# Optimization experiments

Measured on AMD Instinct MI355X. Metric: run time of the kernel, lower is better.

Reference implementation:

```python
import jax, jax.numpy as jnp
import numpy as np

HEAD_SIZE = 64


def setup_inputs() -> dict:
    key = jax.random.key(0)
    k1, k2, k3, k4 = jax.random.split(key, 4)
    B, T, C = 4, 4096, 1024
    x = jax.random.normal(k1, (B, T, C), dtype=jnp.float32)
    s = 1.0 / np.sqrt(C)  # ~kaiming-uniform scale for Linear weights
    Wk = jax.random.normal(k2, (C, HEAD_SIZE), dtype=jnp.float32) * s
    Wq = jax.random.normal(k3, (C, HEAD_SIZE), dtype=jnp.float32) * s
    Wv = jax.random.normal(k4, (C, HEAD_SIZE), dtype=jnp.float32) * s
    return {"x": x, "Wk": Wk, "Wq": Wq, "Wv": Wv}


def reference(x, Wk, Wq, Wv):
    # x: [B,T,C]; Wk/Wq/Wv: [C,H]
    B, T, C = x.shape
    H = Wk.shape[1]
    k = jnp.einsum('btc,ch->bth', x, Wk)
    q = jnp.einsum('btc,ch->bth', x, Wq)
    v = jnp.einsum('btc,ch->bth', x, Wv)
    scale = 1.0 / jnp.sqrt(jnp.asarray(H, dtype=x.dtype))
    scores = jnp.einsum('bqh,bkh->bqk', q, k) * scale  # [B,T,T]
    causal = jnp.tril(jnp.ones((T, T), dtype=bool))
    scores = jnp.where(causal, scores, jnp.asarray(-jnp.inf, dtype=scores.dtype))
    attn = jax.nn.softmax(scores, axis=-1)
    out = jnp.einsum('bqk,bkh->bqh', attn, v)  # [B,T,H]
    return out
```

## Files before the change

kernel.cpp:

```cpp
#include <hip/hip_runtime.h>
#include <hip/hip_bf16.h>

#define T_ 4096
#define C_ 1024
#define H_ 64
#define LSTR 72
#define XBS 1032

typedef short bf16x8 __attribute__((ext_vector_type(8)));
typedef float f32x4 __attribute__((ext_vector_type(4)));

__device__ __forceinline__ short f2bf(float f) {
  union { __hip_bfloat16 h; short s; } u;
  u.h = __float2bfloat16(f);
  return u.s;
}
__device__ __forceinline__ unsigned pack2(float a, float b) {
  return ((unsigned)(unsigned short)f2bf(b) << 16) | (unsigned short)f2bf(a);
}

__device__ __forceinline__ void stage16(const __hip_bfloat16* g,
                                        __hip_bfloat16* l) {
  __builtin_amdgcn_global_load_lds(
      (const __attribute__((address_space(1))) unsigned*)g,
      (__attribute__((address_space(3))) unsigned*)l, 16, 0, 0);
}

__global__ void wtrans_kernel(const float* __restrict__ Wk,
                              const float* __restrict__ Wq,
                              const float* __restrict__ Wv,
                              __hip_bfloat16* __restrict__ Wtf) {
  int tid = blockIdx.x * 256 + threadIdx.x;
  const int j = tid & 7;
  const int lane = (tid >> 3) & 63;
  const int m = lane & 15;
  const int quad = lane >> 4;
  const int f = (tid >> 9) & 15;
  const int nt = f & 3;
  const int ks = f >> 2;
  const int c = (tid >> 13) & 7;
  const int which = tid >> 16;
  const float* W = (which == 0) ? Wk : ((which == 1) ? Wq : Wv);
  const int cc = c * 128 + ks * 32 + quad * 8 + j;
  const int h = nt * 16 + m;
  Wtf[tid] = __float2bfloat16(W[cc * 64 + h]);
}

__global__ __launch_bounds__(256) void proj_kernel(
    const float* __restrict__ x, const __hip_bfloat16* __restrict__ Wtf,
    __hip_bfloat16* __restrict__ qb, __hip_bfloat16* __restrict__ Kf,
    __hip_bfloat16* __restrict__ Vf) {
  __shared__ __hip_bfloat16 Xb[16 * XBS];
  const int tid = threadIdx.x;
  const int lane = tid & 63;
  const int wave = tid >> 6;
  const int m = lane & 15;
  const int quad = lane >> 4;
  const int t0 = blockIdx.x * 16;

  const float4* xtile = (const float4*)(x + (size_t)t0 * C_);
  float4 xv[16];
#pragma unroll
  for (int k = 0; k < 16; ++k) xv[k] = xtile[tid + k * 256];
#pragma unroll
  for (int k = 0; k < 16; ++k) {
    const int idx = tid + k * 256;
    const int row = idx >> 8;
    const int c4 = idx & 255;
    uint2 u = {pack2(xv[k].x, xv[k].y), pack2(xv[k].z, xv[k].w)};
    *(uint2*)(&Xb[row * XBS + c4 * 4]) = u;
  }
  __syncthreads();

  int whichs[3], ntls[3];
  const __hip_bfloat16* wb[3];
#pragma unroll
  for (int i = 0; i < 3; ++i) {
    const int g = wave * 3 + i;
    whichs[i] = g >> 2;
    ntls[i] = g & 3;
    wb[i] = Wtf + (size_t)whichs[i] * 65536 + ntls[i] * 512 + lane * 8;
  }
  f32x4 acc[3];
#pragma unroll
  for (int i = 0; i < 3; ++i) acc[i] = (f32x4){0.f, 0.f, 0.f, 0.f};

#pragma unroll
  for (int c = 0; c < 8; ++c) {
    bf16x8 bq[12];
#pragma unroll
    for (int i = 0; i < 3; ++i)
#pragma unroll
      for (int ks = 0; ks < 4; ++ks)
        bq[i * 4 + ks] = *(const bf16x8*)(wb[i] + (c * 16 + ks * 4) * 512);
#pragma unroll
    for (int ks = 0; ks < 4; ++ks) {
      bf16x8 a = *(const bf16x8*)(&Xb[m * XBS + c * 128 + ks * 32 + quad * 8]);
#pragma unroll
      for (int i = 0; i < 3; ++i)
        acc[i] = __builtin_amdgcn_mfma_f32_16x16x32_bf16(a, bq[i * 4 + ks],
                                                         acc[i], 0, 0, 0);
    }
  }

  const int bb = t0 >> 12;
  const int tloc = t0 & (T_ - 1);
  const int ktile = tloc >> 6;
  const float cscale = 0.18033688011112042f;

#pragma unroll
  for (int i = 0; i < 3; ++i) {
    const int which = whichs[i];
    const int ntl = ntls[i];
    if (which == 1) {
#pragma unroll
      for (int r = 0; r < 4; ++r)
        qb[(size_t)(t0 + quad * 4 + r) * H_ + ntl * 16 + m] =
            __float2bfloat16(acc[i][r] * cscale);
    } else if (which == 0) {
      __hip_bfloat16* dst = Kf + ((size_t)bb * 64 + ktile) * 4096;
      const int ntK = (tloc >> 4) & 3;
      const int wh = ntl >> 1;
      const int quadK = (ntl * 2 + (m >> 3)) & 3;
      const int j = m & 7;
#pragma unroll
      for (int r = 0; r < 4; ++r) {
        const int mK = quad * 4 + r;
        dst[(ntK * 2 + wh) * 512 + (quadK * 16 + mK) * 8 + j] =
            __float2bfloat16(acc[i][r]);
      }
    } else {
      __hip_bfloat16* dst = Vf + ((size_t)bb * 64 + ktile) * 4096;
#pragma unroll
      for (int r = 0; r < 4; ++r) {
        const int kvo = (tloc & 63) + quad * 4 + r;
        const int half = (kvo >> 5) & 1;
        const int quadV = (kvo >> 3) & 3;
        const int j = kvo & 7;
        dst[(ntl * 2 + half) * 512 + (quadV * 16 + m) * 8 + j] =
            __float2bfloat16(acc[i][r]);
      }
    }
  }
}

__global__ __launch_bounds__(256, 4) void fa_pass1(
    const __hip_bfloat16* __restrict__ qg, const __hip_bfloat16* __restrict__ Kf,
    const __hip_bfloat16* __restrict__ Vf, float* __restrict__ Opart,
    float* __restrict__ Ml) {
  __shared__ __align__(16) __hip_bfloat16 KV[8192];
  __shared__ __hip_bfloat16 Pl[4][16 * LSTR];
  const int lane = threadIdx.x & 63;
  const int wave = threadIdx.x >> 6;
  const int m = lane & 15;
  const int quad = lane >> 4;

  const int sid = 1151 - (int)blockIdx.x;
  const int b = sid / 288;
  const int rem = sid - b * 288;
  int g = 7;
  while (4 * g * (g + 1) > rem) --g;
  const int t = rem - 4 * g * (g + 1);
  const int qq = t / (g + 1);
  const int c = t - qq * (g + 1);
  const int Q = 8 * g + qq;
  const int qt = 4 * Q + wave;
  const int q0 = qt * 16;
  const int jid = b * 1152 + 16 * g * (g + 1) + (4 * qq + wave) * (g + 1) + c;
  const int kt0 = 8 * c;
  const int kcR = Q - 8 * c + 1;
  const int kcount = (kcR < 8) ? kcR : 8;

  const __hip_bfloat16* qbase = qg + ((size_t)b * T_ + q0 + m) * H_;
  bf16x8 qf0 = *(const bf16x8*)(qbase + quad * 8);
  bf16x8 qf1 = *(const bf16x8*)(qbase + 32 + quad * 8);

  f32x4 Oacc[4];
#pragma unroll
  for (int i = 0; i < 4; ++i) Oacc[i] = (f32x4){0.f, 0.f, 0.f, 0.f};
  float psum = 0.f;

  const __hip_bfloat16* Kb = Kf + (size_t)b * 262144;
  const __hip_bfloat16* Vb = Vf + (size_t)b * 262144;
  __hip_bfloat16* Plw = &Pl[wave][0];

  for (int it = 0; it < kcount; ++it) {
    const int ktile = kt0 + it;
    const int k0 = ktile * 64;
    const __hip_bfloat16* kp = Kb + (size_t)ktile * 4096;
    const __hip_bfloat16* vp = Vb + (size_t)ktile * 4096;

    __syncthreads();
#pragma unroll
    for (int i = 0; i < 4; ++i) {
      const int idx = wave * 4 + i;
      const __hip_bfloat16* src =
          (idx < 8) ? (kp + idx * 512) : (vp + (idx - 8) * 512);
      stage16(src + lane * 8, &KV[idx * 512]);
    }
    __syncthreads();

    f32x4 s[4];
#pragma unroll
    for (int nt = 0; nt < 4; ++nt) {
      bf16x8 kf0 = *(const bf16x8*)(&KV[nt * 1024 + lane * 8]);
      bf16x8 kf1 = *(const bf16x8*)(&KV[nt * 1024 + 512 + lane * 8]);
      f32x4 tt = (f32x4){0.f, 0.f, 0.f, 0.f};
      tt = __builtin_amdgcn_mfma_f32_16x16x32_bf16(kf0, qf0, tt, 0, 0, 0);
      tt = __builtin_amdgcn_mfma_f32_16x16x32_bf16(kf1, qf1, tt, 0, 0, 0);
      s[nt] = tt;
    }
    bf16x8 vf[8];
#pragma unroll
    for (int nt = 0; nt < 4; ++nt) {
      vf[2 * nt] = *(const bf16x8*)(&KV[4096 + nt * 1024 + lane * 8]);
      vf[2 * nt + 1] = *(const bf16x8*)(&KV[4096 + nt * 1024 + 512 + lane * 8]);
    }

    const bool needmask = (k0 + 63 > q0);
#pragma unroll
    for (int nt = 0; nt < 4; ++nt) {
      float p[4];
#pragma unroll
      for (int r = 0; r < 4; ++r) {
        float sv = s[nt][r];
        if (needmask && (k0 + nt * 16 + quad * 4 + r) > (q0 + m))
          sv = -__builtin_inff();
        p[r] = exp2f(sv);
        psum += p[r];
      }
      uint2 u = {pack2(p[0], p[1]), pack2(p[2], p[3])};
      *(uint2*)(&Plw[m * LSTR + nt * 16 + quad * 4]) = u;
    }

    bf16x8 pf0 = *(const bf16x8*)(&Plw[m * LSTR + quad * 8]);
    bf16x8 pf1 = *(const bf16x8*)(&Plw[m * LSTR + 32 + quad * 8]);
#pragma unroll
    for (int nt = 0; nt < 4; ++nt) {
      Oacc[nt] = __builtin_amdgcn_mfma_f32_16x16x32_bf16(pf0, vf[2 * nt], Oacc[nt], 0, 0, 0);
      Oacc[nt] = __builtin_amdgcn_mfma_f32_16x16x32_bf16(pf1, vf[2 * nt + 1], Oacc[nt], 0, 0, 0);
    }
  }

  psum += __shfl_xor(psum, 16);
  psum += __shfl_xor(psum, 32);

  float* Op = Opart + (size_t)jid * 1024;
#pragma unroll
  for (int nt = 0; nt < 4; ++nt)
#pragma unroll
    for (int r = 0; r < 4; ++r)
      Op[(quad * 4 + r) * 64 + nt * 16 + m] = Oacc[nt][r];
  if (lane < 16) Ml[(size_t)jid * 16 + lane] = psum;
}

__global__ __launch_bounds__(256) void fa_combine(
    const float* __restrict__ Opart, const float* __restrict__ Ml,
    float* __restrict__ out) {
  const int bq = blockIdx.x;
  const int b = bq >> 8;
  const int qt = bq & 255;
  const int g = qt >> 5;
  const int nc = g + 1;
  const int jbase = b * 1152 + 16 * g * (g + 1) + (qt & 31) * nc;
  const int r = threadIdx.x >> 4;
  const int h0 = (threadIdx.x & 15) * 4;

  float4 O = {0.f, 0.f, 0.f, 0.f};
  float L = 0.f;
  for (int c = 0; c < nc; ++c) {
    L += Ml[(size_t)(jbase + c) * 16 + r];
    float4 o = *(const float4*)(Opart + (size_t)(jbase + c) * 1024 + r * 64 + h0);
    O.x += o.x; O.y += o.y; O.z += o.z; O.w += o.w;
  }
  float inv = 1.f / L;
  float4 res = {O.x * inv, O.y * inv, O.z * inv, O.w * inv};
  *(float4*)(out + ((size_t)b * T_ + qt * 16 + r) * H_ + h0) = res;
}

extern "C" void kernel_launch(void* const* d_in, const int* in_sizes, int n_in,
                              void* d_out, int out_size, void* d_ws, size_t ws_size,
                              hipStream_t stream) {
  const float* x = (const float*)d_in[0];
  const float* Wk = (const float*)d_in[1];
  const float* Wq = (const float*)d_in[2];
  const float* Wv = (const float*)d_in[3];
  float* out = (float*)d_out;
  char* ws = (char*)d_ws;
  __hip_bfloat16* Wtf = (__hip_bfloat16*)ws;
  __hip_bfloat16* qb = (__hip_bfloat16*)(ws + 393216);
  __hip_bfloat16* Kf = (__hip_bfloat16*)(ws + 2490368);
  __hip_bfloat16* Vf = (__hip_bfloat16*)(ws + 4587520);
  float* Opart = (float*)(ws + 6684672);
  float* Ml = (float*)(ws + 25559040);

  hipLaunchKernelGGL(wtrans_kernel, dim3(768), dim3(256), 0, stream, Wk, Wq, Wv, Wtf);
  hipLaunchKernelGGL(proj_kernel, dim3(1024), dim3(256), 0, stream, x, Wtf, qb, Kf, Vf);
  hipLaunchKernelGGL(fa_pass1, dim3(1152), dim3(256), 0, stream, qb, Kf, Vf, Opart, Ml);
  hipLaunchKernelGGL(fa_combine, dim3(1024), dim3(256), 0, stream, Opart, Ml, out);
}
```

Before: 144.3 us.

## Fuse split-K combine into attention pass via atomic last-block reduction

Removes the separate combine kernel. Each attention wave writes its partial output and row sum, then bumps a per-query-tile atomic counter, and the last arriving wave sums all chunks, normalises and writes the final output. Tiles with a single chunk write normalised output directly and skip the partial buffer. This saves one kernel launch and a partial round-trip for single-chunk tiles, at the cost of fences, atomics, counter zeroing in the weight-transpose kernel, and a serial tail reduction done by one wave.

```diff
diff --git a/kernel.cpp b/kernel.cpp
--- a/kernel.cpp
+++ b/kernel.cpp
@@ -29,8 +29,10 @@
 __global__ void wtrans_kernel(const float* __restrict__ Wk,
                               const float* __restrict__ Wq,
                               const float* __restrict__ Wv,
-                              __hip_bfloat16* __restrict__ Wtf) {
+                              __hip_bfloat16* __restrict__ Wtf,
+                              int* __restrict__ ctr) {
   int tid = blockIdx.x * 256 + threadIdx.x;
+  if (tid < 1024) ctr[tid] = 0;
   const int j = tid & 7;
   const int lane = (tid >> 3) & 63;
   const int m = lane & 15;
@@ -147,7 +149,7 @@
 __global__ __launch_bounds__(256, 4) void fa_pass1(
     const __hip_bfloat16* __restrict__ qg, const __hip_bfloat16* __restrict__ Kf,
     const __hip_bfloat16* __restrict__ Vf, float* __restrict__ Opart,
-    float* __restrict__ Ml) {
+    float* __restrict__ Ml, int* __restrict__ ctr, float* __restrict__ out) {
   __shared__ __align__(16) __hip_bfloat16 KV[8192];
   __shared__ __hip_bfloat16 Pl[4][16 * LSTR];
   const int lane = threadIdx.x & 63;
@@ -166,7 +168,9 @@
   const int Q = 8 * g + qq;
   const int qt = 4 * Q + wave;
   const int q0 = qt * 16;
-  const int jid = b * 1152 + 16 * g * (g + 1) + (4 * qq + wave) * (g + 1) + c;
+  const int nc = g + 1;
+  const int jbase = b * 1152 + 16 * g * (g + 1) + (4 * qq + wave) * nc;
+  const int jid = jbase + c;
   const int kt0 = 8 * c;
   const int kcR = Q - 8 * c + 1;
   const int kcount = (kcR < 8) ? kcR : 8;
@@ -245,37 +249,61 @@
   psum += __shfl_xor(psum, 16);
   psum += __shfl_xor(psum, 32);
 
-  float* Op = Opart + (size_t)jid * 1024;
-#pragma unroll
-  for (int nt = 0; nt < 4; ++nt)
-#pragma unroll
-    for (int r = 0; r < 4; ++r)
-      Op[(quad * 4 + r) * 64 + nt * 16 + m] = Oacc[nt][r];
-  if (lane < 16) Ml[(size_t)jid * 16 + lane] = psum;
-}
-
-__global__ __launch_bounds__(256) void fa_combine(
-    const float* __restrict__ Opart, const float* __restrict__ Ml,
-    float* __restrict__ out) {
-  const int bq = blockIdx.x;
-  const int b = bq >> 8;
-  const int qt = bq & 255;
-  const int g = qt >> 5;
-  const int nc = g + 1;
-  const int jbase = b * 1152 + 16 * g * (g + 1) + (qt & 31) * nc;
-  const int r = threadIdx.x >> 4;
-  const int h0 = (threadIdx.x & 15) * 4;
-
-  float4 O = {0.f, 0.f, 0.f, 0.f};
-  float L = 0.f;
-  for (int c = 0; c < nc; ++c) {
-    L += Ml[(size_t)(jbase + c) * 16 + r];
-    float4 o = *(const float4*)(Opart + (size_t)(jbase + c) * 1024 + r * 64 + h0);
-    O.x += o.x; O.y += o.y; O.z += o.z; O.w += o.w;
-  }
-  float inv = 1.f / L;
-  float4 res = {O.x * inv, O.y * inv, O.z * inv, O.w * inv};
-  *(float4*)(out + ((size_t)b * T_ + qt * 16 + r) * H_ + h0) = res;
+  if (nc == 1) {
+    float Lr[4];
+#pragma unroll
+    for (int r = 0; r < 4; ++r) Lr[r] = __shfl(psum, quad * 4 + r);
+#pragma unroll
+    for (int nt = 0; nt < 4; ++nt)
+#pragma unroll
+      for (int r = 0; r < 4; ++r)
+        out[((size_t)b * T_ + q0 + quad * 4 + r) * H_ + nt * 16 + m] =
+            Oacc[nt][r] / Lr[r];
+  } else {
+    float* Op = Opart + (size_t)jid * 1024;
+#pragma unroll
+    for (int nt = 0; nt < 4; ++nt)
+#pragma unroll
+      for (int r = 0; r < 4; ++r)
+        Op[(quad * 4 + r) * 64 + nt * 16 + m] = Oacc[nt][r];
+    if (lane < 16) Ml[(size_t)jid * 16 + lane] = psum;
+
+    __threadfence();
+    int old = 0;
+    if (lane == 0) old = atomicAdd(&ctr[b * 256 + qt], 1);
+    old = __shfl(old, 0);
+    if (old == nc - 1) {
+      __threadfence();
+      float4 O[4];
+      float Lr[4];
+#pragma unroll
+      for (int k = 0; k < 4; ++k) O[k] = (float4){0.f, 0.f, 0.f, 0.f};
+      for (int c2 = 0; c2 < nc; ++c2) {
+        const float* Opc = Opart + (size_t)(jbase + c2) * 1024;
+#pragma unroll
+        for (int k = 0; k < 4; ++k) {
+          float4 o = *(const float4*)(Opc + (lane + k * 64) * 4);
+          O[k].x += o.x; O[k].y += o.y; O[k].z += o.z; O[k].w += o.w;
+        }
+      }
+#pragma unroll
+      for (int k = 0; k < 4; ++k) {
+        const int row = (lane + k * 64) >> 4;
+        float L = 0.f;
+        for (int c2 = 0; c2 < nc; ++c2) L += Ml[(size_t)(jbase + c2) * 16 + row];
+        Lr[k] = L;
+      }
+#pragma unroll
+      for (int k = 0; k < 4; ++k) {
+        const int idx4 = lane + k * 64;
+        const int row = idx4 >> 4;
+        const int c4 = idx4 & 15;
+        const float inv = 1.f / Lr[k];
+        float4 res = {O[k].x * inv, O[k].y * inv, O[k].z * inv, O[k].w * inv};
+        *(float4*)(out + ((size_t)b * T_ + qt * 16 + row) * H_ + c4 * 4) = res;
+      }
+    }
+  }
 }
 
 extern "C" void kernel_launch(void* const* d_in, const int* in_sizes, int n_in,
@@ -293,9 +321,12 @@
   __hip_bfloat16* Vf = (__hip_bfloat16*)(ws + 4587520);
   float* Opart = (float*)(ws + 6684672);
   float* Ml = (float*)(ws + 25559040);
-
-  hipLaunchKernelGGL(wtrans_kernel, dim3(768), dim3(256), 0, stream, Wk, Wq, Wv, Wtf);
-  hipLaunchKernelGGL(proj_kernel, dim3(1024), dim3(256), 0, stream, x, Wtf, qb, Kf, Vf);
-  hipLaunchKernelGGL(fa_pass1, dim3(1152), dim3(256), 0, stream, qb, Kf, Vf, Opart, Ml);
-  hipLaunchKernelGGL(fa_combine, dim3(1024), dim3(256), 0, stream, Opart, Ml, out);
-}
+  int* ctr = (int*)(ws + 25853952);
+
+  hipLaunchKernelGGL(wtrans_kernel, dim3(768), dim3(256), 0, stream, Wk, Wq, Wv,
+                     Wtf, ctr);
+  hipLaunchKernelGGL(proj_kernel, dim3(1024), dim3(256), 0, stream, x, Wtf, qb,
+                     Kf, Vf);
+  hipLaunchKernelGGL(fa_pass1, dim3(1152), dim3(256), 0, stream, qb, Kf, Vf,
+                     Opart, Ml, ctr, out);
+}
```

New measurement: 337.3 us. +133.7%, slower.

## Double-buffer K tiles in LDS and read V directly from global

Applied to the files above, without the earlier changes.

Replaces the single combined K/V LDS buffer with a two-slot K buffer. The next K tile is prefetched asynchronously while the current one is used, which cuts the loop to one barrier per iteration. V fragments are now loaded straight from global memory by every wave rather than staged through LDS, and the occupancy hint rises from 4 to 5 blocks. The trade-offs: the same V tile is fetched redundantly by all four waves through the cache, and the V loads share the vmcnt counter with the K prefetch, so waiting on V may also stall on the prefetch and limit the overlap.

```diff
diff --git a/kernel.cpp b/kernel.cpp
--- a/kernel.cpp
+++ b/kernel.cpp
@@ -144,11 +144,11 @@
   }
 }
 
-__global__ __launch_bounds__(256, 4) void fa_pass1(
+__global__ __launch_bounds__(256, 5) void fa_pass1(
     const __hip_bfloat16* __restrict__ qg, const __hip_bfloat16* __restrict__ Kf,
     const __hip_bfloat16* __restrict__ Vf, float* __restrict__ Opart,
     float* __restrict__ Ml) {
-  __shared__ __align__(16) __hip_bfloat16 KV[8192];
+  __shared__ __align__(16) __hip_bfloat16 Kl[2][4096];
   __shared__ __hip_bfloat16 Pl[4][16 * LSTR];
   const int lane = threadIdx.x & 63;
   const int wave = threadIdx.x >> 6;
@@ -181,40 +181,51 @@
   float psum = 0.f;
 
   const __hip_bfloat16* Kb = Kf + (size_t)b * 262144;
-  const __hip_bfloat16* Vb = Vf + (size_t)b * 262144;
+  const __hip_bfloat16* vgf = Vf + (size_t)b * 262144 + lane * 8;
   __hip_bfloat16* Plw = &Pl[wave][0];
+
+  __hip_bfloat16* Kcur = &Kl[0][0];
+  __hip_bfloat16* Knxt = &Kl[1][0];
+
+  {
+    const __hip_bfloat16* kp = Kb + (size_t)kt0 * 4096;
+#pragma unroll
+    for (int i = 0; i < 2; ++i) {
+      const int idx = wave * 2 + i;
+      stage16(kp + idx * 512 + lane * 8, Kcur + idx * 512);
+    }
+  }
 
   for (int it = 0; it < kcount; ++it) {
     const int ktile = kt0 + it;
     const int k0 = ktile * 64;
-    const __hip_bfloat16* kp = Kb + (size_t)ktile * 4096;
-    const __hip_bfloat16* vp = Vb + (size_t)ktile * 4096;
-
     __syncthreads();
-#pragma unroll
-    for (int i = 0; i < 4; ++i) {
-      const int idx = wave * 4 + i;
-      const __hip_bfloat16* src =
-          (idx < 8) ? (kp + idx * 512) : (vp + (idx - 8) * 512);
-      stage16(src + lane * 8, &KV[idx * 512]);
-    }
-    __syncthreads();
+
+    if (it + 1 < kcount) {
+      const __hip_bfloat16* kp = Kb + (size_t)(ktile + 1) * 4096;
+#pragma unroll
+      for (int i = 0; i < 2; ++i) {
+        const int idx = wave * 2 + i;
+        stage16(kp + idx * 512 + lane * 8, Knxt + idx * 512);
+      }
+    }
 
     f32x4 s[4];
 #pragma unroll
     for (int nt = 0; nt < 4; ++nt) {
-      bf16x8 kf0 = *(const bf16x8*)(&KV[nt * 1024 + lane * 8]);
-      bf16x8 kf1 = *(const bf16x8*)(&KV[nt * 1024 + 512 + lane * 8]);
+      bf16x8 kf0 = *(const bf16x8*)(Kcur + nt * 1024 + lane * 8);
+      bf16x8 kf1 = *(const bf16x8*)(Kcur + nt * 1024 + 512 + lane * 8);
       f32x4 tt = (f32x4){0.f, 0.f, 0.f, 0.f};
       tt = __builtin_amdgcn_mfma_f32_16x16x32_bf16(kf0, qf0, tt, 0, 0, 0);
       tt = __builtin_amdgcn_mfma_f32_16x16x32_bf16(kf1, qf1, tt, 0, 0, 0);
       s[nt] = tt;
     }
+    const __hip_bfloat16* vp = vgf + (size_t)ktile * 4096;
     bf16x8 vf[8];
 #pragma unroll
     for (int nt = 0; nt < 4; ++nt) {
-      vf[2 * nt] = *(const bf16x8*)(&KV[4096 + nt * 1024 + lane * 8]);
-      vf[2 * nt + 1] = *(const bf16x8*)(&KV[4096 + nt * 1024 + 512 + lane * 8]);
+      vf[2 * nt] = *(const bf16x8*)(vp + nt * 1024);
+      vf[2 * nt + 1] = *(const bf16x8*)(vp + nt * 1024 + 512);
     }
 
     const bool needmask = (k0 + 63 > q0);
@@ -240,6 +251,8 @@
       Oacc[nt] = __builtin_amdgcn_mfma_f32_16x16x32_bf16(pf0, vf[2 * nt], Oacc[nt], 0, 0, 0);
       Oacc[nt] = __builtin_amdgcn_mfma_f32_16x16x32_bf16(pf1, vf[2 * nt + 1], Oacc[nt], 0, 0, 0);
     }
+
+    __hip_bfloat16* tmp = Kcur; Kcur = Knxt; Knxt = tmp;
   }
 
   psum += __shfl_xor(psum, 16);
```

Result: faster. 139.9 us (-3.0%).
